# Performance work log

Measured on AMD Instinct MI355X. Metric: run time of the kernel, lower is better.

The kernel has to match this reference:

```python
import jax, jax.numpy as jnp
import numpy as np

EMBED = 1024  # embed_dim = hidden_dim = out_dim (n_head=1)
NQ, NK = 4096, 4096
NEG = 1e16


def setup_inputs() -> dict:
    key = jax.random.key(0)
    ks = jax.random.split(key, 10)
    stdv = 1.0 / np.sqrt(EMBED)
    lin = lambda kk: jax.random.uniform(kk, (EMBED, EMBED), jnp.float32, -stdv, stdv)
    vec = lambda kk: jax.random.uniform(kk, (EMBED,), jnp.float32, -stdv, stdv)
    return {
        "q": jax.random.normal(ks[0], (NQ, EMBED), jnp.float32),
        "k": jax.random.normal(ks[1], (NK, EMBED), jnp.float32),
        "mask": jax.random.randint(ks[2], (NQ, NK), 0, 2, jnp.int32),
        "wei": jax.random.uniform(ks[3], (NQ, NK), jnp.float32),
        "Wq": lin(ks[4]), "bq": vec(ks[5]),
        "Wk": lin(ks[6]), "bk": vec(ks[7]),
        "Wp": lin(ks[8]), "bp": vec(ks[9]),
    }


def reference(q, k, mask, wei, Wq, bq, Wk, bk, Wp, bp):
    # Linear projections (torch Linear: x @ W.T + b)
    kx = k @ Wk.T + bk                      # [NK, D]
    qx = q @ Wq.T + bq                      # [NQ, D]
    # dot_product score
    score = qx @ kx.T                       # [NQ, NK]
    bias = (mask.astype(jnp.int32) - 1).astype(score.dtype) * NEG
    score = jax.nn.softmax(score + bias, axis=-1)
    # second weighted+masked softmax pass
    score = jax.nn.softmax(score * wei + bias, axis=-1)
    out = (score @ kx) @ Wp.T + bp          # [NQ, D]
    return out, score
```

## Files before the change

### kernel.cpp

```cpp
#include <hip/hip_runtime.h>


typedef __bf16 bf16;
typedef __bf16 bf16x8 __attribute__((ext_vector_type(8)));
typedef __bf16 bf16x4 __attribute__((ext_vector_type(4)));
typedef float  f32x4  __attribute__((ext_vector_type(4)));
typedef float  f32x16 __attribute__((ext_vector_type(16)));
typedef int    i32x4  __attribute__((ext_vector_type(4)));

typedef __attribute__((address_space(1))) void as1_void;
typedef __attribute__((address_space(3))) void as3_void;

#define NQ  4096
#define NKK 4096
#define EMB 1024

#define BM 128
#define BN 128
#define BK 32

__device__ __forceinline__ void gld_lds16(const void* g, void* l) {
    __builtin_amdgcn_global_load_lds((as1_void*)g, (as3_void*)l, 16, 0, 0);
}

#define VWAIT(N) asm volatile("s_waitcnt vmcnt(" #N ")" ::: "memory")
#define CFENCE   asm volatile("" ::: "memory")

__global__ __launch_bounds__(256) void prep_all(
    const float* __restrict__ q, const float* __restrict__ k,
    const float* __restrict__ Wq, const float* __restrict__ Wk, const float* __restrict__ Wp,
    bf16* __restrict__ qh, bf16* __restrict__ ql,
    bf16* __restrict__ kh, bf16* __restrict__ kl,
    bf16* __restrict__ Wqh, bf16* __restrict__ Wql,
    bf16* __restrict__ Wkh, bf16* __restrict__ Wkl,
    bf16* __restrict__ Wph, bf16* __restrict__ Wpl,
    int nqk, int nw)
{
    const int z = blockIdx.y;
    const float* s; bf16* h; bf16* l; int n;
    switch (z) {
        case 0:  s = q;  h = qh;  l = ql;  n = nqk; break;
        case 1:  s = k;  h = kh;  l = kl;  n = nqk; break;
        case 2:  s = Wq; h = Wqh; l = Wql; n = nw;  break;
        case 3:  s = Wk; h = Wkh; l = Wkl; n = nw;  break;
        default: s = Wp; h = Wph; l = Wpl; n = nw;  break;
    }
    const int i = (blockIdx.x * 256 + threadIdx.x) * 4;
    if (i >= n) return;
    f32x4 v = *(const f32x4*)(s + i);
    bf16x4 hv, lv;
#pragma unroll
    for (int c = 0; c < 4; c++) {
        float x = v[c];
        bf16 hh = (bf16)x;
        hv[c] = hh;
        lv[c] = (bf16)(x - (float)hh);
    }
    *(bf16x4*)(h + i) = hv;
    *(bf16x4*)(l + i) = lv;
}

template<int NS, int MODE>
__global__ __launch_bounds__(256) void reduce_k(
    const float* __restrict__ P, const float* __restrict__ bias,
    float* __restrict__ of, bf16* __restrict__ oh, int n, int Nld)
{
    const int i = (blockIdx.x * 256 + threadIdx.x) * 4;
    if (i >= n) return;
    f32x4 v = *(const f32x4*)(P + i);
#pragma unroll
    for (int s = 1; s < NS; s++)
        v += *(const f32x4*)(P + (size_t)s * n + i);
    if (MODE == 1)
        v += *(const f32x4*)(bias + (i & (Nld - 1)));
    if (MODE == 0) {
        bf16x4 o;
#pragma unroll
        for (int c = 0; c < 4; c++) o[c] = (bf16)v[c];
        *(bf16x4*)(oh + i) = o;
    } else {
        *(f32x4*)(of + i) = v;
    }
}

template<int NSPLIT, int HAS_BIAS, int OUT_BF16>
__global__ __launch_bounds__(256) void gemm_bt(
    const bf16* __restrict__ A, const bf16* __restrict__ B,
    const float* __restrict__ bias,
    float* __restrict__ Cf, bf16* __restrict__ Cb,
    int M, int N, int Ksub, int lda, int ldb)
{
    __shared__ bf16 sA[BM * BK];
    __shared__ bf16 sB[BN * BK];
    const int t    = threadIdx.x;
    const int wave = t >> 6;
    const int lane = t & 63;
    const int l31  = lane & 31;
    const int lhi  = lane >> 5;
    const int wm   = wave >> 1;
    const int wn   = wave & 1;
    const int bm   = blockIdx.y * BM;
    const int bn   = blockIdx.x * BN;
    const int srow = t >> 2;
    const int gseg = (t & 3) ^ ((srow >> 1) & 3) ^ ((srow >> 3) & 3);
    const int rsw  = ((l31 >> 1) & 3) ^ ((l31 >> 3) & 3);
    const int kz   = (NSPLIT > 0) ? (int)blockIdx.z : 0;

    A += (size_t)kz * Ksub;
    B += (size_t)kz * Ksub;
    if (NSPLIT > 0) Cf += (size_t)kz * M * N;

    const bf16* ga = A + (size_t)(bm + srow) * lda + gseg * 8;
    const bf16* gb = B + (size_t)(bn + srow) * ldb + gseg * 8;
    char* lA = (char*)sA + wave * 1024;
    char* lB = (char*)sB + wave * 1024;

    f32x16 acc[2][2] = {};

    for (int k0 = 0; k0 < Ksub; k0 += BK) {
        __syncthreads();
        gld_lds16(ga + k0,                      lA);
        gld_lds16(ga + (size_t)64 * lda + k0,   lA + 4096);
        gld_lds16(gb + k0,                      lB);
        gld_lds16(gb + (size_t)64 * ldb + k0,   lB + 4096);
        __syncthreads();
        bf16x8 af[2][2], bfr[2][2];
#pragma unroll
        for (int mi = 0; mi < 2; mi++)
#pragma unroll
            for (int kh = 0; kh < 2; kh++)
                af[mi][kh] = *(const bf16x8*)
                    &sA[(wm * 64 + mi * 32 + l31) * BK + ((kh * 2 + lhi) ^ rsw) * 8];
#pragma unroll
        for (int nj = 0; nj < 2; nj++)
#pragma unroll
            for (int kh = 0; kh < 2; kh++)
                bfr[nj][kh] = *(const bf16x8*)
                    &sB[(wn * 64 + nj * 32 + l31) * BK + ((kh * 2 + lhi) ^ rsw) * 8];
#pragma unroll
        for (int kh = 0; kh < 2; kh++)
#pragma unroll
            for (int mi = 0; mi < 2; mi++)
#pragma unroll
                for (int nj = 0; nj < 2; nj++)
                    acc[mi][nj] = __builtin_amdgcn_mfma_f32_32x32x16_bf16(
                        af[mi][kh], bfr[nj][kh], acc[mi][nj], 0, 0, 0);
    }

#pragma unroll
    for (int mi = 0; mi < 2; mi++)
#pragma unroll
        for (int nj = 0; nj < 2; nj++) {
            const int cg = bn + wn * 64 + nj * 32 + l31;
            const float bv = HAS_BIAS ? bias[cg] : 0.0f;
#pragma unroll
            for (int r = 0; r < 16; r++) {
                const int rg = bm + wm * 64 + mi * 32 + (r & 3) + 8 * (r >> 2) + 4 * lhi;
                const float v = acc[mi][nj][r] + bv;
                const size_t idx = (size_t)rg * N + cg;
                if (NSPLIT > 0)    Cf[idx] = v;
                else if (OUT_BF16) Cb[idx] = (bf16)v;
                else               Cf[idx] = v;
            }
        }
}

template<int BATCH, int HAS_BIAS, int HILO>
__global__ __launch_bounds__(256) void gemm_bt_split(
    const bf16* __restrict__ Ah0, const bf16* __restrict__ Al0,
    const bf16* __restrict__ Bh0, const bf16* __restrict__ Bl0,
    const float* __restrict__ bias0, bf16* __restrict__ Ch0, bf16* __restrict__ Cl0,
    const bf16* __restrict__ Ah1, const bf16* __restrict__ Al1,
    const bf16* __restrict__ Bh1, const bf16* __restrict__ Bl1,
    const float* __restrict__ bias1, bf16* __restrict__ Ch1, bf16* __restrict__ Cl1,
    float* __restrict__ Cf,
    int M, int N, int K)
{
    __shared__ bf16 sAh[BM * BK], sAl[BM * BK], sBh[BN * BK], sBl[BN * BK];
    const int t    = threadIdx.x;
    const int wave = t >> 6;
    const int lane = t & 63;
    const int l31  = lane & 31;
    const int lhi  = lane >> 5;
    const int wm   = wave >> 1;
    const int wn   = wave & 1;
    const int bm   = blockIdx.y * BM;
    const int bn   = blockIdx.x * BN;
    const int srow = t >> 2;
    const int gseg = (t & 3) ^ ((srow >> 1) & 3) ^ ((srow >> 3) & 3);
    const int rsw  = ((l31 >> 1) & 3) ^ ((l31 >> 3) & 3);

    const int mt = BATCH ? (int)blockIdx.z : 0;

    const bf16* Ah = (BATCH && mt) ? Ah1 : Ah0;
    const bf16* Al = (BATCH && mt) ? Al1 : Al0;
    const bf16* Bh = (BATCH && mt) ? Bh1 : Bh0;
    const bf16* Bl = (BATCH && mt) ? Bl1 : Bl0;
    const float* bias = (BATCH && mt) ? bias1 : bias0;
    bf16* Ch = (BATCH && mt) ? Ch1 : Ch0;
    bf16* Cl = (BATCH && mt) ? Cl1 : Cl0;

    const size_t offA = (size_t)(bm + srow) * K + gseg * 8;
    const size_t offB = (size_t)(bn + srow) * K + gseg * 8;
    char* lAh = (char*)sAh + wave * 1024;
    char* lAl = (char*)sAl + wave * 1024;
    char* lBh = (char*)sBh + wave * 1024;
    char* lBl = (char*)sBl + wave * 1024;

    f32x16 acc[2][2] = {};

    for (int k0 = 0; k0 < K; k0 += BK) {
        __syncthreads();
        gld_lds16(Ah + offA + k0,                  lAh);
        gld_lds16(Ah + offA + (size_t)64 * K + k0, lAh + 4096);
        gld_lds16(Al + offA + k0,                  lAl);
        gld_lds16(Al + offA + (size_t)64 * K + k0, lAl + 4096);
        gld_lds16(Bh + offB + k0,                  lBh);
        gld_lds16(Bh + offB + (size_t)64 * K + k0, lBh + 4096);
        gld_lds16(Bl + offB + k0,                  lBl);
        gld_lds16(Bl + offB + (size_t)64 * K + k0, lBl + 4096);
        __syncthreads();
#pragma unroll
        for (int kh = 0; kh < 2; kh++) {
            const int ksw = ((kh * 2 + lhi) ^ rsw) * 8;
            bf16x8 ah[2], al[2], bh2[2], bl2[2];
#pragma unroll
            for (int mi = 0; mi < 2; mi++) {
                const int ro = (wm * 64 + mi * 32 + l31) * BK + ksw;
                ah[mi] = *(const bf16x8*)&sAh[ro];
                al[mi] = *(const bf16x8*)&sAl[ro];
            }
#pragma unroll
            for (int nj = 0; nj < 2; nj++) {
                const int ro = (wn * 64 + nj * 32 + l31) * BK + ksw;
                bh2[nj] = *(const bf16x8*)&sBh[ro];
                bl2[nj] = *(const bf16x8*)&sBl[ro];
            }
#pragma unroll
            for (int mi = 0; mi < 2; mi++)
#pragma unroll
                for (int nj = 0; nj < 2; nj++) {
                    acc[mi][nj] = __builtin_amdgcn_mfma_f32_32x32x16_bf16(al[mi], bh2[nj], acc[mi][nj], 0, 0, 0);
                    acc[mi][nj] = __builtin_amdgcn_mfma_f32_32x32x16_bf16(ah[mi], bl2[nj], acc[mi][nj], 0, 0, 0);
                    acc[mi][nj] = __builtin_amdgcn_mfma_f32_32x32x16_bf16(ah[mi], bh2[nj], acc[mi][nj], 0, 0, 0);
                }
        }
    }

#pragma unroll
    for (int mi = 0; mi < 2; mi++)
#pragma unroll
        for (int nj = 0; nj < 2; nj++) {
            const int cg = bn + wn * 64 + nj * 32 + l31;
            const float bv = HAS_BIAS ? bias[cg] : 0.0f;
#pragma unroll
            for (int r = 0; r < 16; r++) {
                const int rg = bm + wm * 64 + mi * 32 + (r & 3) + 8 * (r >> 2) + 4 * lhi;
                const float v = acc[mi][nj][r] + bv;
                const size_t idx = (size_t)rg * N + cg;
                if (HILO) {
                    const bf16 hh = (bf16)v;
                    Ch[idx] = hh;
                    Cl[idx] = (bf16)(v - (float)hh);
                } else {
                    Cf[idx] = v;
                }
            }
        }
}

__global__ __launch_bounds__(512, 2) void gemm_score256(
    const bf16* __restrict__ Ah, const bf16* __restrict__ Al,
    const bf16* __restrict__ Bh, const bf16* __restrict__ Bl,
    float* __restrict__ Cf,
    const bf16* __restrict__ Wp, const bf16* __restrict__ Kx,
    bf16* __restrict__ kxpT)
{
    __shared__ bf16 smem[65536];
    const int t    = threadIdx.x;
    const int wave = t >> 6;
    const int lane = t & 63;
    const int l31  = lane & 31;
    const int lhi  = lane >> 5;
    const int wm   = wave >> 2;
    const int wn   = wave & 3;
    const int bm   = (blockIdx.x >> 4) * 256;
    const int bn   = (blockIdx.x & 15) * 256;
    const int K    = EMB;

    const int strow = wave * 32 + l31;
    const bf16* gAh = Ah + (size_t)(bm + strow) * K + lhi * 8;
    const bf16* gAl = Al + (size_t)(bm + strow) * K + lhi * 8;
    const bf16* gBh = Bh + (size_t)(bn + strow) * K + lhi * 8;
    const bf16* gBl = Bl + (size_t)(bn + strow) * K + lhi * 8;

    auto stage = [&](int sbB, int tt) {
        char* L = (char*)smem + sbB + wave * 1024;
        const int ko = tt * 16;
        gld_lds16(gAh + ko, L);
        gld_lds16(gAl + ko, L + 8192);
        gld_lds16(gBh + ko, L + 16384);
        gld_lds16(gBl + ko, L + 24576);
    };

    f32x16 acc[4][2] = {};

    const int aoff = wm * 4 * 512 + lhi * 256 + l31 * 8;
    const int boff = 8192 + wn * 2 * 512 + lhi * 256 + l31 * 8;

    auto tile_body = [&](int cbE, int sbB, int stt, bool do_stage) {
        __builtin_amdgcn_s_barrier();
        CFENCE;
        if (do_stage) stage(sbB, stt);
        bf16x8 b_h[2], b_l[2], a_h[4], a_l[4];
#pragma unroll
        for (int nj = 0; nj < 2; nj++) {
            b_h[nj] = *(const bf16x8*)&smem[cbE + boff + nj * 512];
            b_l[nj] = *(const bf16x8*)&smem[cbE + 4096 + boff + nj * 512];
        }
#pragma unroll
        for (int mi = 0; mi < 4; mi++) {
            a_h[mi] = *(const bf16x8*)&smem[cbE + aoff + mi * 512];
            a_l[mi] = *(const bf16x8*)&smem[cbE + 4096 + aoff + mi * 512];
        }
#pragma unroll
        for (int mi = 0; mi < 4; mi++)
#pragma unroll
            for (int nj = 0; nj < 2; nj++) {
                acc[mi][nj] = __builtin_amdgcn_mfma_f32_32x32x16_bf16(a_l[mi], b_h[nj], acc[mi][nj], 0, 0, 0);
                acc[mi][nj] = __builtin_amdgcn_mfma_f32_32x32x16_bf16(a_h[mi], b_l[nj], acc[mi][nj], 0, 0, 0);
                acc[mi][nj] = __builtin_amdgcn_mfma_f32_32x32x16_bf16(a_h[mi], b_h[nj], acc[mi][nj], 0, 0, 0);
            }
    };

    stage(0, 0); stage(32768, 1);

    for (int tb = 0; tb < 60; tb += 4) {
        VWAIT(4); tile_body(    0, 65536, tb + 2, true);
        VWAIT(4); tile_body(16384, 98304, tb + 3, true);
        VWAIT(4); tile_body(32768,     0, tb + 4, true);
        VWAIT(4); tile_body(49152, 32768, tb + 5, true);
    }
    VWAIT(4); tile_body(    0, 65536, 62, true);
    VWAIT(4); tile_body(16384, 98304, 63, true);
    VWAIT(4); tile_body(32768,     0,  0, false);
    VWAIT(0); tile_body(49152,     0,  0, false);

    f32x16 ac2[2] = {};
    {
        const int km  = (blockIdx.x >> 5) * 128;
        const int kn2 = (blockIdx.x & 31) * 128;
        const int wm4 = wave >> 1;
        const int wn2 = wave & 1;
        const bool isW = wave < 4;
        const int wr = (wave & 3) * 32 + l31;
        const bf16* gSrc = isW ? (Wp + (size_t)(km  + wr) * K + lhi * 8)
                               : (Kx + (size_t)(kn2 + wr) * K + lhi * 8);
        const int dstoff = (isW ? 0 : 4096) + (wave & 3) * 1024;
        auto stageK = [&](int bufByte, int tt) {
            gld_lds16(gSrc + tt * 16, (char*)smem + bufByte + dstoff);
        };
        const int avoff = wm4 * 512 + lhi * 256 + l31 * 8;
        const int bvoff = 2048 + wn2 * 2 * 512 + lhi * 256 + l31 * 8;

        auto kbody = [&](int cbE, int bufByte, int stt, bool do_stage) {
            __builtin_amdgcn_s_barrier();
            CFENCE;
            if (do_stage) stageK(bufByte, stt);
            bf16x8 bv0 = *(const bf16x8*)&smem[cbE + bvoff];
            bf16x8 bv1 = *(const bf16x8*)&smem[cbE + bvoff + 512];
            bf16x8 av  = *(const bf16x8*)&smem[cbE + avoff];
            ac2[0] = __builtin_amdgcn_mfma_f32_32x32x16_bf16(av, bv0, ac2[0], 0, 0, 0);
            ac2[1] = __builtin_amdgcn_mfma_f32_32x32x16_bf16(av, bv1, ac2[1], 0, 0, 0);
        };

        stageK(0, 0); stageK(8192, 1);
        for (int tb = 0; tb < 60; tb += 4) {
            VWAIT(1); kbody(    0, 16384, tb + 2, true);
            VWAIT(1); kbody( 4096, 24576, tb + 3, true);
            VWAIT(1); kbody( 8192,     0, tb + 4, true);
            VWAIT(1); kbody(12288,  8192, tb + 5, true);
        }
        VWAIT(1); kbody(    0, 16384, 62, true);
        VWAIT(1); kbody( 4096, 24576, 63, true);
        VWAIT(1); kbody( 8192,     0,  0, false);
        VWAIT(0); kbody(12288,     0,  0, false);

#pragma unroll
        for (int nj = 0; nj < 2; nj++) {
            const int cg = kn2 + wn2 * 64 + nj * 32 + l31;
#pragma unroll
            for (int r = 0; r < 16; r++) {
                const int rg = km + wm4 * 32 + (r & 3) + 8 * (r >> 2) + 4 * lhi;
                kxpT[(size_t)rg * NKK + cg] = (bf16)ac2[nj][r];
            }
        }
    }

#pragma unroll
    for (int mi = 0; mi < 4; mi++)
#pragma unroll
        for (int nj = 0; nj < 2; nj++) {
            const int cg = bn + wn * 64 + nj * 32 + l31;
#pragma unroll
            for (int r = 0; r < 16; r++) {
                const int rg = bm + wm * 128 + mi * 32 + (r & 3) + 8 * (r >> 2) + 4 * lhi;
                Cf[(size_t)rg * NKK + cg] = acc[mi][nj][r];
            }
        }
}

__device__ __forceinline__ float wred_max(float v) {
#pragma unroll
    for (int off = 32; off > 0; off >>= 1) v = fmaxf(v, __shfl_xor(v, off));
    return v;
}
__device__ __forceinline__ float wred_sum(float v) {
#pragma unroll
    for (int off = 32; off > 0; off >>= 1) v += __shfl_xor(v, off);
    return v;
}

__global__ __launch_bounds__(256) void softmax2_kernel(
    float* __restrict__ score, const int* __restrict__ mask,
    const float* __restrict__ wei, bf16* __restrict__ scoreb)
{
    __shared__ float sred[4];
    const int row = blockIdx.x;
    const int t   = threadIdx.x;
    const size_t base = (size_t)row * NKK + (size_t)t * 16;
    const int wv = t >> 6, ln = t & 63;

    float l[16], w[16];
    unsigned mb = 0;
#pragma unroll
    for (int c = 0; c < 4; c++) {
        *(f32x4*)(l + 4 * c) = *(const f32x4*)(score + base + 4 * c);
        *(f32x4*)(w + 4 * c) = *(const f32x4*)(wei + base + 4 * c);
        i32x4 mv = *(const i32x4*)(mask + base + 4 * c);
#pragma unroll
        for (int j = 0; j < 4; j++) if (mv[j] != 0) mb |= 1u << (4 * c + j);
    }

    float mx = -__builtin_inff();
#pragma unroll
    for (int s = 0; s < 16; s++) if (mb & (1u << s)) mx = fmaxf(mx, l[s]);
    mx = wred_max(mx);
    if (ln == 0) sred[wv] = mx;
    __syncthreads();
    mx = fmaxf(fmaxf(sred[0], sred[1]), fmaxf(sred[2], sred[3]));
    __syncthreads();
    float sum = 0.f;
#pragma unroll
    for (int s = 0; s < 16; s++) {
        const float e = (mb & (1u << s)) ? __expf(l[s] - mx) : 0.f;
        l[s] = e; sum += e;
    }
    sum = wred_sum(sum);
    if (ln == 0) sred[wv] = sum;
    __syncthreads();
    sum = sred[0] + sred[1] + sred[2] + sred[3];
    __syncthreads();
    const float inv1 = 1.0f / sum;

#pragma unroll
    for (int s = 0; s < 16; s++) l[s] = l[s] * inv1 * w[s];

    float mx2 = -__builtin_inff();
#pragma unroll
    for (int s = 0; s < 16; s++) if (mb & (1u << s)) mx2 = fmaxf(mx2, l[s]);
    mx2 = wred_max(mx2);
    if (ln == 0) sred[wv] = mx2;
    __syncthreads();
    mx2 = fmaxf(fmaxf(sred[0], sred[1]), fmaxf(sred[2], sred[3]));
    __syncthreads();
    float sum2 = 0.f;
#pragma unroll
    for (int s = 0; s < 16; s++) {
        const float e = (mb & (1u << s)) ? __expf(l[s] - mx2) : 0.f;
        l[s] = e; sum2 += e;
    }
    sum2 = wred_sum(sum2);
    if (ln == 0) sred[wv] = sum2;
    __syncthreads();
    sum2 = sred[0] + sred[1] + sred[2] + sred[3];
    const float inv2 = 1.0f / sum2;

#pragma unroll
    for (int c = 0; c < 4; c++) {
        f32x4 pv;
#pragma unroll
        for (int j = 0; j < 4; j++) pv[j] = l[4 * c + j] * inv2;
        __builtin_nontemporal_store(pv, (f32x4*)(score + base + 4 * c));
#pragma unroll
        for (int j = 0; j < 4; j++) l[4 * c + j] = pv[j];
    }
    bf16x8 b0, b1;
#pragma unroll
    for (int j = 0; j < 8; j++) { b0[j] = (bf16)l[j]; b1[j] = (bf16)l[8 + j]; }
    *(bf16x8*)(scoreb + base)     = b0;
    *(bf16x8*)(scoreb + base + 8) = b1;
}

extern "C" void kernel_launch(void* const* d_in, const int* in_sizes, int n_in,
                              void* d_out, int out_size, void* d_ws, size_t ws_size,
                              hipStream_t stream)
{
    (void)in_sizes; (void)n_in; (void)out_size;
    const float* q    = (const float*)d_in[0];
    const float* k    = (const float*)d_in[1];
    const int*   mask = (const int*)  d_in[2];
    const float* wei  = (const float*)d_in[3];
    const float* Wq   = (const float*)d_in[4];
    const float* bq   = (const float*)d_in[5];
    const float* Wk   = (const float*)d_in[6];
    const float* bk   = (const float*)d_in[7];
    const float* Wp   = (const float*)d_in[8];
    const float* bp   = (const float*)d_in[9];

    float* out   = (float*)d_out;
    float* score = (float*)d_out + (size_t)NQ * EMB;

    char* ws = (char*)d_ws;
    size_t off = 0;
    auto alloc = [&](size_t bytes) -> char* {
        char* p = ws + off; off += (bytes + 255) & ~(size_t)255; return p;
    };
    const size_t n_qk = (size_t)NQ * EMB;
    const size_t n_w  = (size_t)EMB * EMB;
    const size_t n_sc = (size_t)NQ * NKK;

    bf16* qh   = (bf16*)alloc(n_qk * 2);
    bf16* ql   = (bf16*)alloc(n_qk * 2);
    bf16* kh   = (bf16*)alloc(n_qk * 2);
    bf16* kl   = (bf16*)alloc(n_qk * 2);
    bf16* qxh  = (bf16*)alloc(n_qk * 2);
    bf16* qxl  = (bf16*)alloc(n_qk * 2);
    bf16* kxh  = (bf16*)alloc(n_qk * 2);
    bf16* kxl  = (bf16*)alloc(n_qk * 2);
    bf16* Wqh  = (bf16*)alloc(n_w * 2);
    bf16* Wql  = (bf16*)alloc(n_w * 2);
    bf16* Wkh  = (bf16*)alloc(n_w * 2);
    bf16* Wkl  = (bf16*)alloc(n_w * 2);
    bf16* Wpb  = (bf16*)alloc(n_w * 2);
    bf16* Wpl  = (bf16*)alloc(n_w * 2);
    bf16* kxpTb = (bf16*)alloc(n_qk * 2);
    bf16* scoreb = (bf16*)alloc(n_sc * 2);
    const size_t base_off = off;
    float* P = (float*)alloc(2 * n_qk * 4);
    const bool ws_ok = (off <= ws_size);
    if (base_off > ws_size) return;

    const int MN = (int)n_qk;

    prep_all<<<dim3(n_qk / 1024, 5), 256, 0, stream>>>(
        q, k, Wq, Wk, Wp,
        qh, ql, kh, kl, Wqh, Wql, Wkh, Wkl, Wpb, Wpl,
        (int)n_qk, (int)n_w);

    gemm_bt_split<1, 1, 1><<<dim3(EMB / BN, NQ / BM, 2), 256, 0, stream>>>(
        qh, ql, Wqh, Wql, bq, qxh, qxl,
        kh, kl, Wkh, Wkl, bk, kxh, kxl,
        nullptr, NQ, EMB, EMB);

    gemm_score256<<<dim3(256), 512, 0, stream>>>(
        qxh, qxl, kxh, kxl, score, Wpb, kxh, kxpTb);

    softmax2_kernel<<<dim3(NQ), 256, 0, stream>>>(score, mask, wei, scoreb);

    if (ws_ok) {
        gemm_bt<2, 0, 0><<<dim3(EMB / BN, NQ / BM, 2), 256, 0, stream>>>(
            scoreb, kxpTb, nullptr, P, nullptr, NQ, EMB, NKK / 2, NKK, NKK);
        reduce_k<2, 1><<<dim3(MN / 1024), 256, 0, stream>>>(
            P, bp, out, nullptr, MN, EMB);
    } else {
        gemm_bt<0, 1, 0><<<dim3(EMB / BN, NQ / BM), 256, 0, stream>>>(
            scoreb, kxpTb, bp, out, nullptr, NQ, EMB, NKK, NKK, NKK);
    }
}
```

Before: 491.9 us.

## Software-pipeline LDS fragment loads with register double buffering in score GEMM

Restructures the main score GEMM loop and the fused Wp·Kx side GEMM so that LDS fragment reads for the next k-tile go into a second register set while MFMAs run on the current one. Global prefetch depth rises from two to three stages. Launch bounds drop from two blocks per CU to one so the doubled fragment registers fit. The aim is to hide LDS read latency behind MFMA issue, at the cost of halving occupancy.

```diff
diff --git a/kernel.cpp b/kernel.cpp
--- a/kernel.cpp
+++ b/kernel.cpp
@@ -269,7 +269,7 @@
         }
 }
 
-__global__ __launch_bounds__(512, 2) void gemm_score256(
+__global__ __launch_bounds__(512, 1) void gemm_score256(
     const bf16* __restrict__ Ah, const bf16* __restrict__ Al,
     const bf16* __restrict__ Bh, const bf16* __restrict__ Bl,
     float* __restrict__ Cf,
@@ -308,43 +308,70 @@
     const int aoff = wm * 4 * 512 + lhi * 256 + l31 * 8;
     const int boff = 8192 + wn * 2 * 512 + lhi * 256 + l31 * 8;
 
-    auto tile_body = [&](int cbE, int sbB, int stt, bool do_stage) {
-        __builtin_amdgcn_s_barrier();
-        CFENCE;
-        if (do_stage) stage(sbB, stt);
-        bf16x8 b_h[2], b_l[2], a_h[4], a_l[4];
+    bf16x8 Xah[4], Xal[4], Xbh[2], Xbl[2];
+    bf16x8 Yah[4], Yal[4], Ybh[2], Ybl[2];
+
+    auto loadset = [&](bf16x8 (&ah)[4], bf16x8 (&al)[4],
+                       bf16x8 (&bh)[2], bf16x8 (&bl)[2], int cbE) {
 #pragma unroll
         for (int nj = 0; nj < 2; nj++) {
-            b_h[nj] = *(const bf16x8*)&smem[cbE + boff + nj * 512];
-            b_l[nj] = *(const bf16x8*)&smem[cbE + 4096 + boff + nj * 512];
+            bh[nj] = *(const bf16x8*)&smem[cbE + boff + nj * 512];
+            bl[nj] = *(const bf16x8*)&smem[cbE + 4096 + boff + nj * 512];
         }
 #pragma unroll
         for (int mi = 0; mi < 4; mi++) {
-            a_h[mi] = *(const bf16x8*)&smem[cbE + aoff + mi * 512];
-            a_l[mi] = *(const bf16x8*)&smem[cbE + 4096 + aoff + mi * 512];
-        }
+            ah[mi] = *(const bf16x8*)&smem[cbE + aoff + mi * 512];
+            al[mi] = *(const bf16x8*)&smem[cbE + 4096 + aoff + mi * 512];
+        }
+    };
+    auto mfmaset = [&](bf16x8 (&ah)[4], bf16x8 (&al)[4],
+                       bf16x8 (&bh)[2], bf16x8 (&bl)[2]) {
 #pragma unroll
         for (int mi = 0; mi < 4; mi++)
 #pragma unroll
             for (int nj = 0; nj < 2; nj++) {
-                acc[mi][nj] = __builtin_amdgcn_mfma_f32_32x32x16_bf16(a_l[mi], b_h[nj], acc[mi][nj], 0, 0, 0);
-                acc[mi][nj] = __builtin_amdgcn_mfma_f32_32x32x16_bf16(a_h[mi], b_l[nj], acc[mi][nj], 0, 0, 0);
-                acc[mi][nj] = __builtin_amdgcn_mfma_f32_32x32x16_bf16(a_h[mi], b_h[nj], acc[mi][nj], 0, 0, 0);
+                acc[mi][nj] = __builtin_amdgcn_mfma_f32_32x32x16_bf16(al[mi], bh[nj], acc[mi][nj], 0, 0, 0);
+                acc[mi][nj] = __builtin_amdgcn_mfma_f32_32x32x16_bf16(ah[mi], bl[nj], acc[mi][nj], 0, 0, 0);
+                acc[mi][nj] = __builtin_amdgcn_mfma_f32_32x32x16_bf16(ah[mi], bh[nj], acc[mi][nj], 0, 0, 0);
             }
     };
 
-    stage(0, 0); stage(32768, 1);
+    stage(0, 0); stage(32768, 1); stage(65536, 2);
+    VWAIT(8);
+    __builtin_amdgcn_s_barrier();
+    CFENCE;
+    loadset(Xah, Xal, Xbh, Xbl, 0);
 
     for (int tb = 0; tb < 60; tb += 4) {
-        VWAIT(4); tile_body(    0, 65536, tb + 2, true);
-        VWAIT(4); tile_body(16384, 98304, tb + 3, true);
-        VWAIT(4); tile_body(32768,     0, tb + 4, true);
-        VWAIT(4); tile_body(49152, 32768, tb + 5, true);
-    }
-    VWAIT(4); tile_body(    0, 65536, 62, true);
-    VWAIT(4); tile_body(16384, 98304, 63, true);
-    VWAIT(4); tile_body(32768,     0,  0, false);
-    VWAIT(0); tile_body(49152,     0,  0, false);
+        VWAIT(4); __builtin_amdgcn_s_barrier(); CFENCE;
+        stage(98304, tb + 3);
+        loadset(Yah, Yal, Ybh, Ybl, 16384);
+        mfmaset(Xah, Xal, Xbh, Xbl);
+        VWAIT(4); __builtin_amdgcn_s_barrier(); CFENCE;
+        stage(0, tb + 4);
+        loadset(Xah, Xal, Xbh, Xbl, 32768);
+        mfmaset(Yah, Yal, Ybh, Ybl);
+        VWAIT(4); __builtin_amdgcn_s_barrier(); CFENCE;
+        stage(32768, tb + 5);
+        loadset(Yah, Yal, Ybh, Ybl, 49152);
+        mfmaset(Xah, Xal, Xbh, Xbl);
+        VWAIT(4); __builtin_amdgcn_s_barrier(); CFENCE;
+        stage(65536, tb + 6);
+        loadset(Xah, Xal, Xbh, Xbl, 0);
+        mfmaset(Yah, Yal, Ybh, Ybl);
+    }
+    VWAIT(4); __builtin_amdgcn_s_barrier(); CFENCE;
+    stage(98304, 63);
+    loadset(Yah, Yal, Ybh, Ybl, 16384);
+    mfmaset(Xah, Xal, Xbh, Xbl);
+    VWAIT(4); __builtin_amdgcn_s_barrier(); CFENCE;
+    loadset(Xah, Xal, Xbh, Xbl, 32768);
+    mfmaset(Yah, Yal, Ybh, Ybl);
+    VWAIT(0); __builtin_amdgcn_s_barrier(); CFENCE;
+    loadset(Yah, Yal, Ybh, Ybl, 49152);
+    mfmaset(Xah, Xal, Xbh, Xbl);
+    __builtin_amdgcn_s_barrier(); CFENCE;
+    mfmaset(Yah, Yal, Ybh, Ybl);
 
     f32x16 ac2[2] = {};
     {
@@ -363,28 +390,52 @@
         const int avoff = wm4 * 512 + lhi * 256 + l31 * 8;
         const int bvoff = 2048 + wn2 * 2 * 512 + lhi * 256 + l31 * 8;
 
-        auto kbody = [&](int cbE, int bufByte, int stt, bool do_stage) {
-            __builtin_amdgcn_s_barrier();
-            CFENCE;
-            if (do_stage) stageK(bufByte, stt);
-            bf16x8 bv0 = *(const bf16x8*)&smem[cbE + bvoff];
-            bf16x8 bv1 = *(const bf16x8*)&smem[cbE + bvoff + 512];
-            bf16x8 av  = *(const bf16x8*)&smem[cbE + avoff];
-            ac2[0] = __builtin_amdgcn_mfma_f32_32x32x16_bf16(av, bv0, ac2[0], 0, 0, 0);
-            ac2[1] = __builtin_amdgcn_mfma_f32_32x32x16_bf16(av, bv1, ac2[1], 0, 0, 0);
+        bf16x8 Ka, Kb0, Kb1, La, Lb0, Lb1;
+        auto loadK = [&](bf16x8& a, bf16x8& b0, bf16x8& b1, int cbE) {
+            b0 = *(const bf16x8*)&smem[cbE + bvoff];
+            b1 = *(const bf16x8*)&smem[cbE + bvoff + 512];
+            a  = *(const bf16x8*)&smem[cbE + avoff];
         };
-
-        stageK(0, 0); stageK(8192, 1);
+        auto mfK = [&](bf16x8& a, bf16x8& b0, bf16x8& b1) {
+            ac2[0] = __builtin_amdgcn_mfma_f32_32x32x16_bf16(a, b0, ac2[0], 0, 0, 0);
+            ac2[1] = __builtin_amdgcn_mfma_f32_32x32x16_bf16(a, b1, ac2[1], 0, 0, 0);
+        };
+
+        stageK(0, 0); stageK(8192, 1); stageK(16384, 2);
+        VWAIT(2);
+        __builtin_amdgcn_s_barrier();
+        CFENCE;
+        loadK(Ka, Kb0, Kb1, 0);
+
         for (int tb = 0; tb < 60; tb += 4) {
-            VWAIT(1); kbody(    0, 16384, tb + 2, true);
-            VWAIT(1); kbody( 4096, 24576, tb + 3, true);
-            VWAIT(1); kbody( 8192,     0, tb + 4, true);
-            VWAIT(1); kbody(12288,  8192, tb + 5, true);
-        }
-        VWAIT(1); kbody(    0, 16384, 62, true);
-        VWAIT(1); kbody( 4096, 24576, 63, true);
-        VWAIT(1); kbody( 8192,     0,  0, false);
-        VWAIT(0); kbody(12288,     0,  0, false);
+            VWAIT(1); __builtin_amdgcn_s_barrier(); CFENCE;
+            stageK(24576, tb + 3);
+            loadK(La, Lb0, Lb1, 4096);
+            mfK(Ka, Kb0, Kb1);
+            VWAIT(1); __builtin_amdgcn_s_barrier(); CFENCE;
+            stageK(0, tb + 4);
+            loadK(Ka, Kb0, Kb1, 8192);
+            mfK(La, Lb0, Lb1);
+            VWAIT(1); __builtin_amdgcn_s_barrier(); CFENCE;
+            stageK(8192, tb + 5);
+            loadK(La, Lb0, Lb1, 12288);
+            mfK(Ka, Kb0, Kb1);
+            VWAIT(1); __builtin_amdgcn_s_barrier(); CFENCE;
+            stageK(16384, tb + 6);
+            loadK(Ka, Kb0, Kb1, 0);
+            mfK(La, Lb0, Lb1);
+        }
+        VWAIT(1); __builtin_amdgcn_s_barrier(); CFENCE;
+        stageK(24576, 63);
+        loadK(La, Lb0, Lb1, 4096);
+        mfK(Ka, Kb0, Kb1);
+        VWAIT(1); __builtin_amdgcn_s_barrier(); CFENCE;
+        loadK(Ka, Kb0, Kb1, 8192);
+        mfK(La, Lb0, Lb1);
+        VWAIT(0); __builtin_amdgcn_s_barrier(); CFENCE;
+        loadK(La, Lb0, Lb1, 12288);
+        mfK(Ka, Kb0, Kb1);
+        mfK(La, Lb0, Lb1);
 
 #pragma unroll
         for (int nj = 0; nj < 2; nj++) {
```

After: 496.8 us. Within noise of the previous version (+1.0%).

## Deepen score GEMM pipeline to three stages with split-phase MFMA/load interleave

Applied to the files above, without the earlier changes.

The score GEMM main loop now keeps three K-tiles in flight instead of two. Each tile is split into two half-phases: A loads are issued during the first half and B loads during the second, with barriers, s_setprio around the MFMA clusters, and explicit LDS waits. Launch bounds drop from 2 to 1 block per CU, which frees registers but lowers occupancy. The aim is to hide global-to-LDS latency behind MFMA work and to keep waves in step. The cost is extra barriers per tile, and fewer resident waves may leave latency exposed.

```diff
diff --git a/kernel.cpp b/kernel.cpp
--- a/kernel.cpp
+++ b/kernel.cpp
@@ -24,6 +24,7 @@
 }
 
 #define VWAIT(N) asm volatile("s_waitcnt vmcnt(" #N ")" ::: "memory")
+#define LGKM0    asm volatile("s_waitcnt lgkmcnt(0)" ::: "memory")
 #define CFENCE   asm volatile("" ::: "memory")
 
 __global__ __launch_bounds__(256) void prep_all(
@@ -269,7 +270,7 @@
         }
 }
 
-__global__ __launch_bounds__(512, 2) void gemm_score256(
+__global__ __launch_bounds__(512, 1) void gemm_score256(
     const bf16* __restrict__ Ah, const bf16* __restrict__ Al,
     const bf16* __restrict__ Bh, const bf16* __restrict__ Bl,
     float* __restrict__ Cf,
@@ -294,11 +295,15 @@
     const bf16* gBh = Bh + (size_t)(bn + strow) * K + lhi * 8;
     const bf16* gBl = Bl + (size_t)(bn + strow) * K + lhi * 8;
 
-    auto stage = [&](int sbB, int tt) {
+    auto stageA2 = [&](int sbB, int tt) {
         char* L = (char*)smem + sbB + wave * 1024;
         const int ko = tt * 16;
         gld_lds16(gAh + ko, L);
         gld_lds16(gAl + ko, L + 8192);
+    };
+    auto stageB2 = [&](int sbB, int tt) {
+        char* L = (char*)smem + sbB + wave * 1024;
+        const int ko = tt * 16;
         gld_lds16(gBh + ko, L + 16384);
         gld_lds16(gBl + ko, L + 24576);
     };
@@ -308,43 +313,70 @@
     const int aoff = wm * 4 * 512 + lhi * 256 + l31 * 8;
     const int boff = 8192 + wn * 2 * 512 + lhi * 256 + l31 * 8;
 
-    auto tile_body = [&](int cbE, int sbB, int stt, bool do_stage) {
-        __builtin_amdgcn_s_barrier();
-        CFENCE;
-        if (do_stage) stage(sbB, stt);
-        bf16x8 b_h[2], b_l[2], a_h[4], a_l[4];
+    auto chunk_body = [&](int cbE, int sbB, int stt, bool do_stage) {
+        bf16x8 b_h[2], b_l[2], a_h[2], a_l[2];
 #pragma unroll
         for (int nj = 0; nj < 2; nj++) {
             b_h[nj] = *(const bf16x8*)&smem[cbE + boff + nj * 512];
             b_l[nj] = *(const bf16x8*)&smem[cbE + 4096 + boff + nj * 512];
         }
 #pragma unroll
-        for (int mi = 0; mi < 4; mi++) {
-            a_h[mi] = *(const bf16x8*)&smem[cbE + aoff + mi * 512];
-            a_l[mi] = *(const bf16x8*)&smem[cbE + 4096 + aoff + mi * 512];
-        }
-#pragma unroll
-        for (int mi = 0; mi < 4; mi++)
+        for (int i = 0; i < 2; i++) {
+            a_h[i] = *(const bf16x8*)&smem[cbE + aoff + i * 512];
+            a_l[i] = *(const bf16x8*)&smem[cbE + 4096 + aoff + i * 512];
+        }
+        if (do_stage) stageA2(sbB, stt);
+        __builtin_amdgcn_s_barrier();
+        LGKM0;
+        __builtin_amdgcn_sched_barrier(0);
+        __builtin_amdgcn_s_setprio(1);
+#pragma unroll
+        for (int i = 0; i < 2; i++)
 #pragma unroll
             for (int nj = 0; nj < 2; nj++) {
-                acc[mi][nj] = __builtin_amdgcn_mfma_f32_32x32x16_bf16(a_l[mi], b_h[nj], acc[mi][nj], 0, 0, 0);
-                acc[mi][nj] = __builtin_amdgcn_mfma_f32_32x32x16_bf16(a_h[mi], b_l[nj], acc[mi][nj], 0, 0, 0);
-                acc[mi][nj] = __builtin_amdgcn_mfma_f32_32x32x16_bf16(a_h[mi], b_h[nj], acc[mi][nj], 0, 0, 0);
-            }
+                acc[i][nj] = __builtin_amdgcn_mfma_f32_32x32x16_bf16(a_l[i], b_h[nj], acc[i][nj], 0, 0, 0);
+                acc[i][nj] = __builtin_amdgcn_mfma_f32_32x32x16_bf16(a_h[i], b_l[nj], acc[i][nj], 0, 0, 0);
+                acc[i][nj] = __builtin_amdgcn_mfma_f32_32x32x16_bf16(a_h[i], b_h[nj], acc[i][nj], 0, 0, 0);
+            }
+        __builtin_amdgcn_s_setprio(0);
+        __builtin_amdgcn_s_barrier();
+        bf16x8 c_h[2], c_l[2];
+#pragma unroll
+        for (int i = 0; i < 2; i++) {
+            c_h[i] = *(const bf16x8*)&smem[cbE + aoff + (2 + i) * 512];
+            c_l[i] = *(const bf16x8*)&smem[cbE + 4096 + aoff + (2 + i) * 512];
+        }
+        if (do_stage) stageB2(sbB, stt);
+        __builtin_amdgcn_s_barrier();
+        LGKM0;
+        __builtin_amdgcn_sched_barrier(0);
+        __builtin_amdgcn_s_setprio(1);
+#pragma unroll
+        for (int i = 0; i < 2; i++)
+#pragma unroll
+            for (int nj = 0; nj < 2; nj++) {
+                acc[2 + i][nj] = __builtin_amdgcn_mfma_f32_32x32x16_bf16(c_l[i], b_h[nj], acc[2 + i][nj], 0, 0, 0);
+                acc[2 + i][nj] = __builtin_amdgcn_mfma_f32_32x32x16_bf16(c_h[i], b_l[nj], acc[2 + i][nj], 0, 0, 0);
+                acc[2 + i][nj] = __builtin_amdgcn_mfma_f32_32x32x16_bf16(c_h[i], b_h[nj], acc[2 + i][nj], 0, 0, 0);
+            }
+        __builtin_amdgcn_s_setprio(0);
+        __builtin_amdgcn_s_barrier();
     };
 
-    stage(0, 0); stage(32768, 1);
+    stageA2(0, 0);     stageB2(0, 0);
+    stageA2(32768, 1); stageB2(32768, 1);
+    stageA2(65536, 2); stageB2(65536, 2);
 
     for (int tb = 0; tb < 60; tb += 4) {
-        VWAIT(4); tile_body(    0, 65536, tb + 2, true);
-        VWAIT(4); tile_body(16384, 98304, tb + 3, true);
-        VWAIT(4); tile_body(32768,     0, tb + 4, true);
-        VWAIT(4); tile_body(49152, 32768, tb + 5, true);
-    }
-    VWAIT(4); tile_body(    0, 65536, 62, true);
-    VWAIT(4); tile_body(16384, 98304, 63, true);
-    VWAIT(4); tile_body(32768,     0,  0, false);
-    VWAIT(0); tile_body(49152,     0,  0, false);
+        VWAIT(8); CFENCE; chunk_body(    0,  98304, tb + 3, true);
+        VWAIT(8); CFENCE; chunk_body(16384,      0, tb + 4, true);
+        VWAIT(8); CFENCE; chunk_body(32768,  32768, tb + 5, true);
+        VWAIT(8); CFENCE; chunk_body(49152,  65536, tb + 6, true);
+    }
+    VWAIT(8); CFENCE; chunk_body(    0,  98304, 63, true);
+    VWAIT(8); CFENCE; chunk_body(16384,      0,  0, false);
+    VWAIT(4); CFENCE; chunk_body(32768,      0,  0, false);
+    VWAIT(0); CFENCE; chunk_body(49152,      0,  0, false);
 
     f32x16 ac2[2] = {};
     {
```

Result: no change. 497.5 us (+1.1%).
